# Kernel tuning notes

Hardware: AMD Instinct MI355X
Metric: run time of the kernel (lower is better)

Reference implementation:

```python
import jax, jax.numpy as jnp
import numpy as np

D_MODEL = 256
D_STATE = 64
D_CONV = 4
EXPAND = 2
HEADDIM = 128
CHUNK = 128
D_INNER = EXPAND * D_MODEL            # 512
NHEADS = D_INNER // HEADDIM           # 4
CONV_DIM = D_INNER + 2 * D_STATE      # 640
D_IN_PROJ = 2 * D_INNER + 2 * D_STATE + NHEADS  # 1156
B = 4
H_IMG, W_IMG = 256, 512


def setup_inputs() -> dict:
    key = jax.random.key(0)
    ks = jax.random.split(key, 8)
    rng = np.random.default_rng(0)
    # dt_bias init as in Mamba2: inverse-softplus of dt ~ logU(dt_min, dt_max)
    dt = np.exp(rng.uniform(size=NHEADS) * (np.log(0.1) - np.log(0.001)) + np.log(0.001))
    inv_dt = (dt + np.log(-np.expm1(-dt))).astype(np.float32)
    A_log = np.log(rng.uniform(1.0, 16.0, size=NHEADS)).astype(np.float32)
    return {
        "left_img": jax.random.normal(ks[0], (B, 3, H_IMG, W_IMG), jnp.float32),
        "right_img": jax.random.normal(ks[1], (B, 3, H_IMG, W_IMG), jnp.float32),
        "downsample_w": jax.random.normal(ks[2], (D_MODEL, 3, 4, 4), jnp.float32) * 0.1,
        "downsample_b": jnp.zeros((D_MODEL,), jnp.float32),
        "in_proj_w": jax.random.normal(ks[3], (D_IN_PROJ, D_MODEL), jnp.float32) * (1.0 / np.sqrt(D_MODEL)),
        "conv_w": jax.random.normal(ks[4], (CONV_DIM, 1, D_CONV), jnp.float32) * 0.2,
        "conv_b": jnp.zeros((CONV_DIM,), jnp.float32),
        "dt_bias": jnp.asarray(inv_dt),
        "A_log": jnp.asarray(A_log),
        "D": jnp.ones((NHEADS,), jnp.float32),
        "norm_w": jnp.ones((D_INNER,), jnp.float32),
        "out_proj_w": jax.random.normal(ks[5], (D_MODEL, D_INNER), jnp.float32) * (1.0 / np.sqrt(D_INNER)),
    }


def _ssd_chunk_scan(x, dt, A, Bm, Cm, D):
    """Mamba2 SSD chunked selective scan.
    x: (b,L,H,P), dt: (b,L,H), A: (H,), Bm/Cm: (b,L,N) (ngroups=1), D: (H,).
    Recurrence: h_t = exp(A*dt_t) h_{t-1} + dt_t B_t x_t^T ; y_t = C_t h_t + D x_t.
    """
    b, L, H, P = x.shape
    N = Bm.shape[-1]
    nc = L // CHUNK
    x_ = x.reshape(b, nc, CHUNK, H, P)
    dt_ = dt.reshape(b, nc, CHUNK, H)
    B_ = Bm.reshape(b, nc, CHUNK, N)
    C_ = Cm.reshape(b, nc, CHUNK, N)
    a = dt_ * A                                   # (b,nc,Q,H)
    cum = jnp.cumsum(a, axis=2)                   # (b,nc,Q,H)
    # intra-chunk (causal) contribution
    seg = cum[:, :, :, None, :] - cum[:, :, None, :, :]   # (b,nc,Q,Q,H)
    tril = jnp.tril(jnp.ones((CHUNK, CHUNK), bool))
    Lmat = jnp.where(tril[None, None, :, :, None], jnp.exp(seg), 0.0)
    CB = jnp.einsum('bcin,bcjn->bcij', C_, B_)
    scores = CB[..., None] * Lmat * dt_[:, :, None, :, :]  # (b,nc,Q,Q,H)
    y = jnp.einsum('bcijh,bcjhp->bcihp', scores, x_)
    # per-chunk end states
    decay_to_end = jnp.exp(cum[:, :, -1:, :] - cum)        # (b,nc,Q,H)
    states = jnp.einsum('bcjn,bcjh,bcjhp->bchpn', B_, dt_ * decay_to_end, x_)
    chunk_decay = jnp.exp(cum[:, :, -1, :])                # (b,nc,H)
    def step(hprev, inp):
        dec, st = inp
        hnew = hprev * dec[:, :, None, None] + st
        return hnew, hprev  # emit state BEFORE this chunk
    h0 = jnp.zeros((b, H, P, N), x.dtype)
    _, hprevs = jax.lax.scan(step, h0, (jnp.moveaxis(chunk_decay, 1, 0), jnp.moveaxis(states, 1, 0)))
    hprev = jnp.moveaxis(hprevs, 0, 1)                     # (b,nc,H,P,N)
    y = y + jnp.einsum('bcin,bcih,bchpn->bcihp', C_, jnp.exp(cum), hprev)
    y = y + D[None, None, None, :, None] * x_
    return y.reshape(b, L, H, P)


def reference(left_img, right_img, downsample_w, downsample_b, in_proj_w, conv_w,
              conv_b, dt_bias, A_log, D, norm_w, out_proj_w):
    def downsample(img):
        y = jax.lax.conv_general_dilated(img, downsample_w, (4, 4), 'VALID',
                                         dimension_numbers=('NCHW', 'OIHW', 'NCHW'))
        return y + downsample_b[None, :, None, None]

    ld = downsample(left_img)   # (b, d_model, 64, 128)
    rd = downsample(right_img)
    b, c, h, w = ld.shape
    L = h * w
    lf = ld.transpose(0, 2, 3, 1).reshape(b, L, c)
    rf = rd.transpose(0, 2, 3, 1).reshape(b, L, c)

    zxl = lf @ in_proj_w.T
    zxr = rf @ in_proj_w.T

    def split_proj(zx):
        z = zx[..., :D_INNER]
        xBC = zx[..., D_INNER:D_INNER + CONV_DIM]
        dt = jax.nn.softplus(zx[..., D_INNER + CONV_DIM:] + dt_bias)
        return z, xBC, dt

    zl, xBCl, dtl = split_proj(zxl)
    zr, xBCr, dtr = split_proj(zxr)

    # causal depthwise conv + SiLU applied to LEFT stream only (as in source)
    xt = xBCl.transpose(0, 2, 1)  # (b, conv_dim, L)
    yt = jax.lax.conv_general_dilated(xt, conv_w, (1,), [(D_CONV - 1, 0)],
                                      dimension_numbers=('NCH', 'OIH', 'NCH'),
                                      feature_group_count=CONV_DIM)
    xBCl = jax.nn.silu((yt + conv_b[None, :, None]).transpose(0, 2, 1))

    def split_xbc(xBC):
        return (xBC[..., :D_INNER],
                xBC[..., D_INNER:D_INNER + D_STATE],
                xBC[..., D_INNER + D_STATE:])

    xl, Bl, Cl = split_xbc(xBCl)
    xr, Br, Cr = split_xbc(xBCr)

    A = -jnp.exp(A_log)
    heads = lambda x: x.reshape(b, L, NHEADS, HEADDIM)
    # cross-mixed scans (faithful to source)
    yl = _ssd_chunk_scan(heads(xr), dtl, A, Br, Cl, D).reshape(b, L, D_INNER)
    yr = _ssd_chunk_scan(heads(xl), dtr, A, Bl, Cr, D).reshape(b, L, D_INNER)

    def gated_rmsnorm(y, z):
        y = y * jax.nn.silu(z)
        return y * jax.lax.rsqrt(jnp.mean(y * y, axis=-1, keepdims=True) + 1e-5) * norm_w

    out_l = (gated_rmsnorm(yl, zl) @ out_proj_w.T).reshape(b, h, w, c)
    out_r = (gated_rmsnorm(yr, zr) @ out_proj_w.T).reshape(b, h, w, c)
    return out_l, out_r
```

## Files before the change

### kernel.cpp

```cpp
#include <hip/hip_runtime.h>
#include <hip/hip_fp16.h>
#include <math.h>


typedef _Float16 f16;
typedef __attribute__((ext_vector_type(8))) _Float16 f16x8;
typedef __attribute__((ext_vector_type(4))) _Float16 f16x4;
typedef __attribute__((ext_vector_type(4))) float f32x4;

__device__ __forceinline__ float fexpf(float v) { return __expf(v); }
__device__ __forceinline__ float siluf(float v) { return v / (1.0f + __expf(-v)); }

__device__ __forceinline__ void gload_lds16(const void* g, void* l) {
    __builtin_amdgcn_global_load_lds(
        (const __attribute__((address_space(1))) void*)g,
        (__attribute__((address_space(3))) void*)l, 16, 0, 0);
}

__global__ __launch_bounds__(256) void k_cvt(
    const float* __restrict__ s, f16* __restrict__ d, int n)
{
    int i = blockIdx.x * 256 + threadIdx.x;
    if (i < n) d[i] = (f16)s[i];
}

__global__ __launch_bounds__(256) void k_downsample(
    const float* __restrict__ limg, const float* __restrict__ rimg,
    const float* __restrict__ w, const float* __restrict__ bias,
    f16* __restrict__ F)
{
    __shared__ float wS[12288];
    __shared__ float pS[768];
    int t = threadIdx.x;
    int bid = blockIdx.x;
    int og = bid & 7;
    int oy = (bid >> 3) & 63;
    int b  = (bid >> 9) & 3;
    int side = bid >> 11;
    const float* img = side ? rimg : limg;

    for (int e = t * 4; e < 12288; e += 1024)
        *(float4*)(wS + e) = *(const float4*)(w + e);

    int ox0 = og * 16;
    for (int f = t; f < 768; f += 256) {
        int kx = f & 3, pix = (f >> 2) & 15, ky = (f >> 6) & 3, ci = f >> 8;
        float v = img[((b * 3 + ci) * 256 + oy * 4 + ky) * 512 + ox0 * 4 + pix * 4 + kx];
        pS[pix * 48 + ci * 16 + ky * 4 + kx] = v;
    }
    __syncthreads();

    int c = t;
    float wreg[48];
#pragma unroll
    for (int q = 0; q < 12; q++) {
        float4 v = *(const float4*)(wS + c * 48 + q * 4);
        wreg[q * 4 + 0] = v.x; wreg[q * 4 + 1] = v.y;
        wreg[q * 4 + 2] = v.z; wreg[q * 4 + 3] = v.w;
    }
    float bv = bias[c];
    long base = ((long)(side * 32768 + b * 8192 + oy * 128 + ox0)) * 256 + c;
    for (int pix = 0; pix < 16; pix++) {
        float acc = bv;
#pragma unroll
        for (int q = 0; q < 12; q++) {
            float4 p4 = *(const float4*)(pS + pix * 48 + q * 4);
            acc += wreg[q * 4 + 0] * p4.x + wreg[q * 4 + 1] * p4.y
                 + wreg[q * 4 + 2] * p4.z + wreg[q * 4 + 3] * p4.w;
        }
        F[base + (long)pix * 256] = (f16)acc;
    }
}

template<typename TO>
__global__ __launch_bounds__(256) void k_gemm_mfma(
    const f16* __restrict__ A, const f16* __restrict__ B,
    TO* __restrict__ CL, TO* __restrict__ CR, int K, int ldc, int split)
{
    __shared__ f16 As[128 * 64];
    __shared__ f16 Bs[128 * 64];
    int t = threadIdx.x;
    int w = t >> 6, lane = t & 63;
    int wm = w >> 1, wn = w & 1;

    int gx = gridDim.x, gy = gridDim.y;
    int nwg = gx * gy;
    int orig = blockIdx.y * gx + blockIdx.x;
    int swz = (orig & 7) * (nwg >> 3) + (orig >> 3);
    int mt, nt;
    if (gx <= gy) { mt = swz % gx; nt = swz / gx; }
    else          { nt = swz % gy; mt = swz / gy; }
    long m0 = (long)mt * 128;
    int n0 = nt * 128;

    f32x4 acc[4][4] = {};

    const f16* ga = A + (m0 + w * 8 + (lane >> 3)) * K + (lane & 7) * 8;
    const f16* gb = B + ((long)n0 + w * 8 + (lane >> 3)) * K + (lane & 7) * 8;
    f16* la = As + (w * 8) * 64;
    f16* lb = Bs + (w * 8) * 64;

    for (int kk = 0; kk < K; kk += 64) {
#pragma unroll
        for (int i = 0; i < 4; i++) {
            gload_lds16(ga + (long)i * 32 * K + kk, la + i * 32 * 64);
            gload_lds16(gb + (long)i * 32 * K + kk, lb + i * 32 * 64);
        }
        __syncthreads();

        const f16* pa = As + (wm * 64 + (lane & 15)) * 64 + (lane >> 4) * 8;
        const f16* pb = Bs + (wn * 64 + (lane & 15)) * 64 + (lane >> 4) * 8;
#pragma unroll
        for (int kb = 0; kb < 2; kb++) {
            f16x8 af[4], bf[4];
#pragma unroll
            for (int r = 0; r < 4; r++)
                af[r] = *(const f16x8*)(pa + r * 16 * 64 + kb * 32);
#pragma unroll
            for (int cn = 0; cn < 4; cn++)
                bf[cn] = *(const f16x8*)(pb + cn * 16 * 64 + kb * 32);
#pragma unroll
            for (int r = 0; r < 4; r++)
#pragma unroll
                for (int cn = 0; cn < 4; cn++)
                    acc[r][cn] = __builtin_amdgcn_mfma_f32_16x16x32_f16(
                        af[r], bf[cn], acc[r][cn], 0, 0, 0);
        }
        __syncthreads();
    }

    int rb = (lane >> 4) * 4;
    int cb = lane & 15;
#pragma unroll
    for (int r = 0; r < 4; r++) {
        long mrow = m0 + wm * 64 + r * 16 + rb;
#pragma unroll
        for (int reg = 0; reg < 4; reg++) {
            long row = mrow + reg;
            TO* Cp = (row < split) ? CL + row * ldc : CR + (row - split) * ldc;
#pragma unroll
            for (int cn = 0; cn < 4; cn++)
                Cp[n0 + wn * 64 + cn * 16 + cb] = (TO)acc[r][cn][reg];
        }
    }
}

__global__ __launch_bounds__(256) void k_dt(
    const f16* __restrict__ F, const float* __restrict__ W,
    const float* __restrict__ dt_bias, float* __restrict__ dtbuf)
{
    int t = threadIdx.x;
    int wv = t >> 6, lane = t & 63;
    long m = (long)blockIdx.x * 4 + wv;
    f16x4 fv = *(const f16x4*)(F + m * 256 + lane * 4);
    float dots[4];
#pragma unroll
    for (int h = 0; h < 4; h++) {
        float4 w4 = *(const float4*)(W + (long)(1152 + h) * 256 + lane * 4);
        float d = (float)fv[0] * w4.x + (float)fv[1] * w4.y
                + (float)fv[2] * w4.z + (float)fv[3] * w4.w;
#pragma unroll
        for (int off = 32; off; off >>= 1) d += __shfl_down(d, off, 64);
        dots[h] = d;
    }
    if (lane == 0) {
        long sb = m >> 13;
        long l = m & 8191;
#pragma unroll
        for (int h = 0; h < 4; h++) {
            float v = dots[h] + dt_bias[h];
            float sp = (v > 20.0f) ? v : log1pf(expf(v));
            dtbuf[(sb * 4 + h) * 8192 + l] = sp;
        }
    }
}

__global__ __launch_bounds__(256) void k_cum(
    const float* __restrict__ dtbuf, const float* __restrict__ A_log,
    float* __restrict__ cumbuf, float* __restrict__ wbuf)
{
    int wv = threadIdx.x >> 6, lane = threadIdx.x & 63;
    int g = blockIdx.x * 4 + wv;
    int c = g & 63, h = (g >> 6) & 3, sb = g >> 8;
    float A = -__expf(A_log[h]);
    long base = ((long)sb * 4 + h) * 8192 + c * 128;
    float2 d = *(const float2*)(dtbuf + base + lane * 2);
    float a0 = d.x * A;
    float p = a0 + d.y * A;
    float s = p;
#pragma unroll
    for (int off = 1; off < 64; off <<= 1) {
        float v = __shfl_up(s, off, 64);
        if (lane >= off) s += v;
    }
    float excl = s - p;
    float c0 = excl + a0, c1 = excl + p;
    float cl = __shfl(s, 63, 64);
    *(float2*)(cumbuf + base + lane * 2) = make_float2(c0, c1);
    *(float2*)(wbuf + base + lane * 2) =
        make_float2(d.x * __expf(cl - c0), d.y * __expf(cl - c1));
}

__global__ __launch_bounds__(256) void k_conv_x(
    const f16* __restrict__ xT, const float* __restrict__ cw,
    const float* __restrict__ cb, f16* __restrict__ XCt)
{
    int bid = blockIdx.x;
    int c = bid >> 4;
    int b = (bid >> 2) & 3;
    int tile = bid & 3;
    int l0 = tile * 2048 + threadIdx.x * 8;
    const f16* row = xT + (long)c * 65536 + b * 8192;
    float w0 = cw[c * 4 + 0], w1 = cw[c * 4 + 1],
          w2 = cw[c * 4 + 2], w3 = cw[c * 4 + 3];
    float bv = cb[c];
    float xv[11];
    f16x8 v = *(const f16x8*)(row + l0);
#pragma unroll
    for (int q = 0; q < 8; q++) xv[3 + q] = (float)v[q];
    if (l0 > 0) {
        xv[0] = (float)row[l0 - 3];
        xv[1] = (float)row[l0 - 2];
        xv[2] = (float)row[l0 - 1];
    } else { xv[0] = xv[1] = xv[2] = 0.f; }
    f16x8 o;
#pragma unroll
    for (int q = 0; q < 8; q++) {
        float acc = bv + w0 * xv[q] + w1 * xv[q + 1] + w2 * xv[q + 2] + w3 * xv[q + 3];
        o[q] = (f16)siluf(acc);
    }
    *(f16x8*)(XCt + (long)c * 32768 + b * 8192 + l0) = o;
}

__global__ __launch_bounds__(256) void k_conv_bc(
    const f16* __restrict__ bcLr, const float* __restrict__ cw,
    const float* __restrict__ cb, f16* __restrict__ bcL)
{
    long idx = (long)blockIdx.x * 256 + threadIdx.x;
    int n = (int)(idx & 127);
    long m = idx >> 7;
    int l = (int)(m & 8191);
    float acc = cb[512 + n];
#pragma unroll
    for (int k = 0; k < 4; k++) {
        int j = l - 3 + k;
        if (j >= 0) acc += cw[(512 + n) * 4 + k] * (float)bcLr[(m - 3 + k) * 128 + n];
    }
    bcL[m * 128 + n] = (f16)siluf(acc);
}

__global__ __launch_bounds__(256) void k_ssd_a(
    const f16* __restrict__ xT, const f16* __restrict__ XCt,
    const f16* __restrict__ bcR, const f16* __restrict__ bcL,
    const float* __restrict__ dtbuf, const float* __restrict__ cumbuf,
    const float* __restrict__ wbuf, const float* __restrict__ Dvec,
    f16* __restrict__ ybuf, f16* __restrict__ states)
{
    extern __shared__ f16 sm[];
    f16* Xs = sm;
    f16* Cs = sm + 16384;
    f16* Bs = sm + 24576;
    f16* Ms = sm + 16384;

    int t = threadIdx.x;
    int w = t >> 6, lane = t & 63;
    int quad = lane >> 4, l16 = lane & 15;
    int wm = w >> 1, wn = w & 1;
    int bid = blockIdx.x;
    int side = bid >> 10, rem = bid & 1023;
    int b = rem >> 8, c = (rem >> 2) & 63, h = rem & 3;
    long l0 = (long)b * 8192 + c * 128;
    long dtbase = ((long)(side * 4 + b) * 4 + h) * 8192 + c * 128;

    const f16* Xg; long ldx;
    const f16 *Bg, *Cg;
    if (side == 0) {
        Xg = xT + (long)(h * 128) * 65536 + 32768 + l0; ldx = 65536;
        Bg = bcR + l0 * 128;
        Cg = bcL + l0 * 128 + 64;
    } else {
        Xg = XCt + (long)(h * 128) * 32768 + l0;        ldx = 32768;
        Bg = bcL + l0 * 128;
        Cg = bcR + l0 * 128 + 64;
    }

    int sw8 = l16 & 7;

#pragma unroll
    for (int q = 0; q < 8; q++) {
        int r0 = w * 32 + q * 4;
        int R = r0 + quad;
        gload_lds16(Xg + (long)R * ldx + ((l16 ^ (R & 7)) << 3), Xs + r0 * 128);
    }
#pragma unroll
    for (int q = 0; q < 4; q++) {
        int r0 = w * 32 + q * 8;
        int R = r0 + (lane >> 3);
        int cc = ((lane & 7) ^ (R & 7)) << 3;
        gload_lds16(Cg + (long)R * 128 + cc, Cs + r0 * 64);
        gload_lds16(Bg + (long)R * 128 + cc, Bs + r0 * 64);
    }

    float cum_i[16], cum_j[4], dt_j[4];
#pragma unroll
    for (int r = 0; r < 4; r++)
#pragma unroll
        for (int reg = 0; reg < 4; reg++)
            cum_i[r * 4 + reg] = cumbuf[dtbase + wm * 64 + r * 16 + quad * 4 + reg];
#pragma unroll
    for (int cn = 0; cn < 4; cn++) {
        int j = wn * 64 + cn * 16 + l16;
        cum_j[cn] = cumbuf[dtbase + j];
        dt_j[cn] = dtbuf[dtbase + j];
    }
    float Dh = Dvec[h];
    __syncthreads();

    f32x4 g[4][4] = {};
#pragma unroll
    for (int kb = 0; kb < 2; kb++) {
        f16x8 af[4], bf[4];
#pragma unroll
        for (int r = 0; r < 4; r++)
            af[r] = *(const f16x8*)(Cs + (wm * 64 + r * 16 + l16) * 64
                                       + (((quad + kb * 4) ^ sw8) << 3));
#pragma unroll
        for (int cn = 0; cn < 4; cn++)
            bf[cn] = *(const f16x8*)(Bs + (wn * 64 + cn * 16 + l16) * 64
                                        + (((quad + kb * 4) ^ sw8) << 3));
#pragma unroll
        for (int r = 0; r < 4; r++)
#pragma unroll
            for (int cn = 0; cn < 4; cn++)
                g[r][cn] = __builtin_amdgcn_mfma_f32_16x16x32_f16(
                    af[r], bf[cn], g[r][cn], 0, 0, 0);
    }
    __syncthreads();

#pragma unroll
    for (int r = 0; r < 4; r++)
#pragma unroll
        for (int cn = 0; cn < 4; cn++)
#pragma unroll
            for (int reg = 0; reg < 4; reg++) {
                int i = wm * 64 + r * 16 + quad * 4 + reg;
                int j = wn * 64 + cn * 16 + l16;
                float v = 0.f;
                if (i >= j)
                    v = g[r][cn][reg] * fexpf(cum_i[r * 4 + reg] - cum_j[cn]) * dt_j[cn];
                if (i == j) v += Dh;
                Ms[i * 128 + ((((j >> 3) ^ (i & 7))) << 3) + (j & 7)] = (f16)v;
            }
    __syncthreads();

    f32x4 y[4][4] = {};
#pragma unroll
    for (int kb = 0; kb < 4; kb++) {
        f16x8 af[4], bf[4];
#pragma unroll
        for (int r = 0; r < 4; r++)
            af[r] = *(const f16x8*)(Ms + (wm * 64 + r * 16 + l16) * 128
                                       + (((quad + kb * 4) ^ sw8) << 3));
#pragma unroll
        for (int cn = 0; cn < 4; cn++)
            bf[cn] = *(const f16x8*)(Xs + (wn * 64 + cn * 16 + l16) * 128
                                        + (((quad + kb * 4) ^ sw8) << 3));
#pragma unroll
        for (int r = 0; r < 4; r++)
#pragma unroll
            for (int cn = 0; cn < 4; cn++)
                y[r][cn] = __builtin_amdgcn_mfma_f32_16x16x32_f16(
                    af[r], bf[cn], y[r][cn], 0, 0, 0);
    }
    long ybase = (long)side * 32768 + l0;
#pragma unroll
    for (int r = 0; r < 4; r++)
#pragma unroll
        for (int reg = 0; reg < 4; reg++) {
            int i = wm * 64 + r * 16 + quad * 4 + reg;
#pragma unroll
            for (int cn = 0; cn < 4; cn++) {
                int p = wn * 64 + cn * 16 + l16;
                ybuf[(ybase + i) * 512 + h * 128 + p] = (f16)y[r][cn][reg];
            }
        }

    f32x4 s[4][2] = {};
#pragma unroll
    for (int kb = 0; kb < 4; kb++) {
        float wj[8];
#pragma unroll
        for (int jj = 0; jj < 8; jj++)
            wj[jj] = wbuf[dtbase + kb * 32 + quad * 8 + jj];
        f16x8 af[4], bf[2];
#pragma unroll
        for (int r = 0; r < 4; r++)
            af[r] = *(const f16x8*)(Xs + (wm * 64 + r * 16 + l16) * 128
                                       + (((quad + kb * 4) ^ sw8) << 3));
#pragma unroll
        for (int cn = 0; cn < 2; cn++) {
            int n = wn * 32 + cn * 16 + l16;
#pragma unroll
            for (int jj = 0; jj < 8; jj++) {
                int j = kb * 32 + quad * 8 + jj;
                bf[cn][jj] = (f16)((float)Bg[(long)j * 128 + n] * wj[jj]);
            }
        }
#pragma unroll
        for (int r = 0; r < 4; r++)
#pragma unroll
            for (int cn = 0; cn < 2; cn++)
                s[r][cn] = __builtin_amdgcn_mfma_f32_16x16x32_f16(
                    af[r], bf[cn], s[r][cn], 0, 0, 0);
    }
    long sbase = (((long)(side * 4 + b) * 64 + c) * 4 + h) * 128;
#pragma unroll
    for (int r = 0; r < 4; r++)
#pragma unroll
        for (int reg = 0; reg < 4; reg++) {
            int p = wm * 64 + r * 16 + quad * 4 + reg;
#pragma unroll
            for (int cn = 0; cn < 2; cn++) {
                int n = wn * 32 + cn * 16 + l16;
                states[(sbase + p) * 64 + n] = (f16)s[r][cn][reg];
            }
        }
}

__global__ __launch_bounds__(256) void k_scan(
    f16* __restrict__ states, const float* __restrict__ cumbuf)
{
    long g = (long)blockIdx.x * 256 + threadIdx.x;
    int n = (int)(g & 63);
    int p = (int)((g >> 6) & 127);
    int h = (int)((g >> 13) & 3);
    int sb = (int)(g >> 15);
    long sbase = (((long)sb * 256 + h) * 128 + p) * 64 + n;
    long cbase = ((long)sb * 4 + h) * 8192 + 127;
    float hr = 0.f;
    for (int c = 0; c < 64; c++) {
        long idx = sbase + (long)c * 32768;
        float dec = fexpf(cumbuf[cbase + (long)c * 128]);
        float sv = (float)states[idx];
        states[idx] = (f16)hr;
        hr = hr * dec + sv;
    }
}

__global__ __launch_bounds__(256) void k_ssd_c(
    const f16* __restrict__ bcR, const f16* __restrict__ bcL,
    const f16* __restrict__ states, const float* __restrict__ cumbuf,
    f16* __restrict__ ybuf)
{
    int t = threadIdx.x;
    int w = t >> 6, lane = t & 63;
    int quad = lane >> 4, l16 = lane & 15;
    int wm = w >> 1, wn = w & 1;
    int bid = blockIdx.x;
    int side = bid >> 10, rem = bid & 1023;
    int b = rem >> 8, c = (rem >> 2) & 63, h = rem & 3;
    long l0 = (long)b * 8192 + c * 128;
    long dtbase = ((long)(side * 4 + b) * 4 + h) * 8192 + c * 128;

    const f16* Cg = (side == 0) ? bcL + l0 * 128 + 64 : bcR + l0 * 128 + 64;
    long stile = (((long)(side * 4 + b) * 64 + c) * 4 + h) * 8192;

    f32x4 acc[4][4] = {};
#pragma unroll
    for (int kb = 0; kb < 2; kb++) {
        f16x8 af[4], bf[4];
#pragma unroll
        for (int r = 0; r < 4; r++)
            af[r] = *(const f16x8*)(Cg + (long)(wm * 64 + r * 16 + l16) * 128 + quad * 8 + kb * 32);
#pragma unroll
        for (int cn = 0; cn < 4; cn++)
            bf[cn] = *(const f16x8*)(states + stile + (long)(wn * 64 + cn * 16 + l16) * 64 + quad * 8 + kb * 32);
#pragma unroll
        for (int r = 0; r < 4; r++)
#pragma unroll
            for (int cn = 0; cn < 4; cn++)
                acc[r][cn] = __builtin_amdgcn_mfma_f32_16x16x32_f16(
                    af[r], bf[cn], acc[r][cn], 0, 0, 0);
    }
    long ybase = (long)side * 32768 + l0;
#pragma unroll
    for (int r = 0; r < 4; r++)
#pragma unroll
        for (int reg = 0; reg < 4; reg++) {
            int i = wm * 64 + r * 16 + quad * 4 + reg;
            float ex = fexpf(cumbuf[dtbase + i]);
            f16* yrow = ybuf + (ybase + i) * 512 + h * 128;
#pragma unroll
            for (int cn = 0; cn < 4; cn++) {
                int p = wn * 64 + cn * 16 + l16;
                yrow[p] = (f16)((float)yrow[p] + ex * acc[r][cn][reg]);
            }
        }
}

__global__ __launch_bounds__(256) void k_rmsnorm(
    __half* __restrict__ ybuf, const __half* __restrict__ zbuf,
    const float* __restrict__ nw)
{
    int t = threadIdx.x;
    int wv = t >> 6, lane = t & 63;
    long r = (long)blockIdx.x * 4 + wv;
    __half2* yrow = (__half2*)(ybuf + r * 512 + lane * 8);
    const __half2* zrow = (const __half2*)(zbuf + r * 512 + lane * 8);
    float g[8];
#pragma unroll
    for (int j = 0; j < 4; j++) {
        float2 yv = __half22float2(yrow[j]);
        float2 zv = __half22float2(zrow[j]);
        g[2 * j]     = yv.x * siluf(zv.x);
        g[2 * j + 1] = yv.y * siluf(zv.y);
    }
    float ss = 0.f;
#pragma unroll
    for (int i = 0; i < 8; i++) ss += g[i] * g[i];
#pragma unroll
    for (int off = 32; off; off >>= 1) ss += __shfl_xor(ss, off, 64);
    float sc = rsqrtf(ss * (1.0f / 512.0f) + 1e-5f);
#pragma unroll
    for (int j = 0; j < 4; j++) {
        float w0 = nw[lane * 8 + 2 * j], w1 = nw[lane * 8 + 2 * j + 1];
        yrow[j] = __floats2half2_rn(g[2 * j] * sc * w0, g[2 * j + 1] * sc * w1);
    }
}

extern "C" void kernel_launch(void* const* d_in, const int* in_sizes, int n_in,
                              void* d_out, int out_size, void* d_ws, size_t ws_size,
                              hipStream_t stream)
{
    (void)in_sizes; (void)n_in; (void)out_size; (void)ws_size;
    const float* limg = (const float*)d_in[0];
    const float* rimg = (const float*)d_in[1];
    const float* dsw  = (const float*)d_in[2];
    const float* dsb  = (const float*)d_in[3];
    const float* ipw  = (const float*)d_in[4];
    const float* cw   = (const float*)d_in[5];
    const float* cb   = (const float*)d_in[6];
    const float* dtb  = (const float*)d_in[7];
    const float* alog = (const float*)d_in[8];
    const float* Dv   = (const float*)d_in[9];
    const float* nw   = (const float*)d_in[10];
    const float* opw  = (const float*)d_in[11];
    float* out = (float*)d_out;

    char* ws = (char*)d_ws;
    f16*   F16    = (f16*)  (ws + 0);
    f16*   ipw16  = (f16*)  (ws + 33554432);
    f16*   opw16  = (f16*)  (ws + 34146304);
    float* dtbuf  = (float*)(ws + 34408448);
    float* cumbuf = (float*)(ws + 35457024);
    float* wbuf   = (float*)(ws + 36505600);
    f16*   xT     = (f16*)  (ws + 37554176);
    f16*   XCt    = (f16*)  (ws + 104663040);
    f16*   bcLr   = (f16*)  (ws + 138217472);
    f16*   bcR    = (f16*)  (ws + 146606080);
    f16*   bcL    = (f16*)  (ws + 154994688);
    f16*   ybuf   = (f16*)  (ws + 163383296);
    f16*   states = (f16*)  (ws + 230492160);
    f16*   zbuf   = xT;

    const int BIG = 1 << 30;
    k_downsample<<<4096, 256, 0, stream>>>(limg, rimg, dsw, dsb, F16);
    k_cvt<<<1156, 256, 0, stream>>>(ipw, ipw16, 1156 * 256);
    k_cvt<<<512, 256, 0, stream>>>(opw, opw16, 256 * 512);
    k_gemm_mfma<f16><<<dim3(512, 1), 256, 0, stream>>>(
        F16, ipw16 + 1024 * 256, bcLr, bcR, 256, 128, 32768);
    k_gemm_mfma<f16><<<dim3(4, 512), 256, 0, stream>>>(
        ipw16 + 512 * 256, F16, xT, xT, 256, 65536, BIG);
    k_dt<<<16384, 256, 0, stream>>>(F16, ipw, dtb, dtbuf);
    k_cum<<<512, 256, 0, stream>>>(dtbuf, alog, cumbuf, wbuf);
    k_conv_x<<<8192, 256, 0, stream>>>(xT, cw, cb, XCt);
    k_conv_bc<<<16384, 256, 0, stream>>>(bcLr, cw, cb, bcL);
    k_ssd_a<<<2048, 256, 65536, stream>>>(
        xT, XCt, bcR, bcL, dtbuf, cumbuf, wbuf, Dv, ybuf, states);
    k_scan<<<1024, 256, 0, stream>>>(states, cumbuf);
    k_ssd_c<<<2048, 256, 0, stream>>>(bcR, bcL, states, cumbuf, ybuf);
    k_gemm_mfma<f16><<<dim3(512, 4), 256, 0, stream>>>(
        F16, ipw16, zbuf, zbuf, 256, 512, BIG);
    k_rmsnorm<<<16384, 256, 0, stream>>>((__half*)ybuf, (__half*)zbuf, nw);
    k_gemm_mfma<float><<<dim3(512, 2), 256, 0, stream>>>(
        ybuf, opw16, out, out + (long)32768 * 256, 512, 256, 32768);
}
```

Baseline: 504.8 us.

## Fuse inter-chunk state output with gated RMSNorm via LDS-resident y tile

Merges the inter-chunk output kernel and the gated RMSNorm kernel. Each block now loads a 64-row by 512-column y tile into swizzled LDS, adds the state contribution for all four heads there, then applies SiLU gating and the RMSNorm before writing y back once. This removes the read-modify-write global passes over y that the two separate kernels made. The scan kernel also preloads all 64 chunk states into registers before running the recurrence, which raises register pressure. The fused kernel needs 64KB of LDS per block and gives each block less parallelism across heads.

After: 559.1 us. +10.8%, slower.

```diff
diff --git a/kernel.cpp b/kernel.cpp
--- a/kernel.cpp
+++ b/kernel.cpp
@@ -437,94 +437,132 @@
     int sb = (int)(g >> 15);
     long sbase = (((long)sb * 256 + h) * 128 + p) * 64 + n;
     long cbase = ((long)sb * 4 + h) * 8192 + 127;
+    float sv[64];
+#pragma unroll
+    for (int c = 0; c < 64; c++)
+        sv[c] = (float)states[sbase + (long)c * 32768];
     float hr = 0.f;
+#pragma unroll
     for (int c = 0; c < 64; c++) {
-        long idx = sbase + (long)c * 32768;
-        float dec = fexpf(cumbuf[cbase + (long)c * 128]);
-        float sv = (float)states[idx];
-        states[idx] = (f16)hr;
-        hr = hr * dec + sv;
-    }
-}
-
-__global__ __launch_bounds__(256) void k_ssd_c(
+        states[sbase + (long)c * 32768] = (f16)hr;
+        hr = hr * fexpf(cumbuf[cbase + (long)c * 128]) + sv[c];
+    }
+}
+
+__global__ __launch_bounds__(256) void k_ssd_cn(
     const f16* __restrict__ bcR, const f16* __restrict__ bcL,
     const f16* __restrict__ states, const float* __restrict__ cumbuf,
+    const f16* __restrict__ zbuf, const float* __restrict__ nw,
     f16* __restrict__ ybuf)
 {
+    extern __shared__ f16 gS[];
     int t = threadIdx.x;
     int w = t >> 6, lane = t & 63;
     int quad = lane >> 4, l16 = lane & 15;
     int wm = w >> 1, wn = w & 1;
     int bid = blockIdx.x;
-    int side = bid >> 10, rem = bid & 1023;
-    int b = rem >> 8, c = (rem >> 2) & 63, h = rem & 3;
-    long l0 = (long)b * 8192 + c * 128;
-    long dtbase = ((long)(side * 4 + b) * 4 + h) * 8192 + c * 128;
-
-    const f16* Cg = (side == 0) ? bcL + l0 * 128 + 64 : bcR + l0 * 128 + 64;
-    long stile = (((long)(side * 4 + b) * 64 + c) * 4 + h) * 8192;
-
-    f32x4 acc[4][4] = {};
-#pragma unroll
-    for (int kb = 0; kb < 2; kb++) {
-        f16x8 af[4], bf[4];
-#pragma unroll
-        for (int r = 0; r < 4; r++)
-            af[r] = *(const f16x8*)(Cg + (long)(wm * 64 + r * 16 + l16) * 128 + quad * 8 + kb * 32);
-#pragma unroll
-        for (int cn = 0; cn < 4; cn++)
-            bf[cn] = *(const f16x8*)(states + stile + (long)(wn * 64 + cn * 16 + l16) * 64 + quad * 8 + kb * 32);
-#pragma unroll
-        for (int r = 0; r < 4; r++)
+    int sb = bid >> 7, c = (bid >> 1) & 63, half = bid & 1;
+    int side = sb >> 2, b = sb & 3;
+    long lrow0 = (long)b * 8192 + c * 128 + half * 64;
+    long grow0 = (long)side * 32768 + lrow0;
+
+    {
+        int row = t >> 2, quarter = t & 3;
+        const f16* src = ybuf + (grow0 + row) * 512 + quarter * 128;
+        f16* dst = gS + row * 512;
+        int sw = (row & 7) << 3;
+#pragma unroll
+        for (int k = 0; k < 16; k++) {
+            int lg = quarter * 16 + k;
+            *(f16x8*)(dst + ((lg ^ sw) << 3)) = *(const f16x8*)(src + k * 8);
+        }
+    }
+    __syncthreads();
+
+    const f16* Cg = ((side == 0) ? bcL : bcR) + lrow0 * 128 + 64;
+    f16x8 af[2][2];
+#pragma unroll
+    for (int r = 0; r < 2; r++)
+#pragma unroll
+        for (int kb = 0; kb < 2; kb++)
+            af[r][kb] = *(const f16x8*)(Cg + (long)(wm * 32 + r * 16 + l16) * 128
+                                           + quad * 8 + kb * 32);
+#pragma unroll
+    for (int h = 0; h < 4; h++) {
+        long stile = (((long)sb * 64 + c) * 4 + h) * 8192;
+        f32x4 acc[2][4] = {};
+#pragma unroll
+        for (int kb = 0; kb < 2; kb++) {
+            f16x8 bf[4];
 #pragma unroll
             for (int cn = 0; cn < 4; cn++)
-                acc[r][cn] = __builtin_amdgcn_mfma_f32_16x16x32_f16(
-                    af[r], bf[cn], acc[r][cn], 0, 0, 0);
-    }
-    long ybase = (long)side * 32768 + l0;
-#pragma unroll
-    for (int r = 0; r < 4; r++)
-#pragma unroll
-        for (int reg = 0; reg < 4; reg++) {
-            int i = wm * 64 + r * 16 + quad * 4 + reg;
-            float ex = fexpf(cumbuf[dtbase + i]);
-            f16* yrow = ybuf + (ybase + i) * 512 + h * 128;
-#pragma unroll
-            for (int cn = 0; cn < 4; cn++) {
-                int p = wn * 64 + cn * 16 + l16;
-                yrow[p] = (f16)((float)yrow[p] + ex * acc[r][cn][reg]);
+                bf[cn] = *(const f16x8*)(states + stile
+                            + (long)(wn * 64 + cn * 16 + l16) * 64 + quad * 8 + kb * 32);
+#pragma unroll
+            for (int r = 0; r < 2; r++)
+#pragma unroll
+                for (int cn = 0; cn < 4; cn++)
+                    acc[r][cn] = __builtin_amdgcn_mfma_f32_16x16x32_f16(
+                        af[r][kb], bf[cn], acc[r][cn], 0, 0, 0);
+        }
+        long dtb = ((long)sb * 4 + h) * 8192 + c * 128 + half * 64;
+#pragma unroll
+        for (int r = 0; r < 2; r++)
+#pragma unroll
+            for (int reg = 0; reg < 4; reg++) {
+                int i = wm * 32 + r * 16 + quad * 4 + reg;
+                float ex = fexpf(cumbuf[dtb + i]);
+                int sw = (i & 7) << 3;
+#pragma unroll
+                for (int cn = 0; cn < 4; cn++) {
+                    int col = h * 128 + wn * 64 + cn * 16 + l16;
+                    int addr = i * 512 + ((((col >> 3) ^ sw)) << 3) + (col & 7);
+                    gS[addr] = (f16)((float)gS[addr] + ex * acc[r][cn][reg]);
+                }
             }
-        }
-}
-
-__global__ __launch_bounds__(256) void k_rmsnorm(
-    __half* __restrict__ ybuf, const __half* __restrict__ zbuf,
-    const float* __restrict__ nw)
-{
-    int t = threadIdx.x;
-    int wv = t >> 6, lane = t & 63;
-    long r = (long)blockIdx.x * 4 + wv;
-    __half2* yrow = (__half2*)(ybuf + r * 512 + lane * 8);
-    const __half2* zrow = (const __half2*)(zbuf + r * 512 + lane * 8);
-    float g[8];
-#pragma unroll
-    for (int j = 0; j < 4; j++) {
-        float2 yv = __half22float2(yrow[j]);
-        float2 zv = __half22float2(zrow[j]);
-        g[2 * j]     = yv.x * siluf(zv.x);
-        g[2 * j + 1] = yv.y * siluf(zv.y);
-    }
-    float ss = 0.f;
-#pragma unroll
-    for (int i = 0; i < 8; i++) ss += g[i] * g[i];
-#pragma unroll
-    for (int off = 32; off; off >>= 1) ss += __shfl_xor(ss, off, 64);
-    float sc = rsqrtf(ss * (1.0f / 512.0f) + 1e-5f);
-#pragma unroll
-    for (int j = 0; j < 4; j++) {
-        float w0 = nw[lane * 8 + 2 * j], w1 = nw[lane * 8 + 2 * j + 1];
-        yrow[j] = __floats2half2_rn(g[2 * j] * sc * w0, g[2 * j + 1] * sc * w1);
+    }
+    __syncthreads();
+
+    {
+        int row = t >> 2, quarter = t & 3;
+        int sw = (row & 7) << 3;
+        long grow = grow0 + row;
+        const f16* zrow = zbuf + grow * 512 + quarter * 128;
+        f16x8 gv[16];
+        float ssq = 0.f;
+#pragma unroll
+        for (int k = 0; k < 16; k++) {
+            int lg = quarter * 16 + k;
+            f16x8 yv = *(const f16x8*)(gS + row * 512 + ((lg ^ sw) << 3));
+            f16x8 zv = *(const f16x8*)(zrow + k * 8);
+            f16x8 gg;
+#pragma unroll
+            for (int q = 0; q < 8; q++) {
+                float gf = (float)yv[q] * siluf((float)zv[q]);
+                gg[q] = (f16)gf;
+                ssq += gf * gf;
+            }
+            gv[k] = gg;
+        }
+        ssq += __shfl_xor(ssq, 1, 64);
+        ssq += __shfl_xor(ssq, 2, 64);
+        float sc = rsqrtf(ssq * (1.0f / 512.0f) + 1e-5f);
+        f16* orow = ybuf + grow * 512 + quarter * 128;
+#pragma unroll
+        for (int k = 0; k < 16; k++) {
+            float4 w0 = *(const float4*)(nw + quarter * 128 + k * 8);
+            float4 w1 = *(const float4*)(nw + quarter * 128 + k * 8 + 4);
+            f16x8 o;
+            o[0] = (f16)((float)gv[k][0] * sc * w0.x);
+            o[1] = (f16)((float)gv[k][1] * sc * w0.y);
+            o[2] = (f16)((float)gv[k][2] * sc * w0.z);
+            o[3] = (f16)((float)gv[k][3] * sc * w0.w);
+            o[4] = (f16)((float)gv[k][4] * sc * w1.x);
+            o[5] = (f16)((float)gv[k][5] * sc * w1.y);
+            o[6] = (f16)((float)gv[k][6] * sc * w1.z);
+            o[7] = (f16)((float)gv[k][7] * sc * w1.w);
+            *(f16x8*)(orow + k * 8) = o;
+        }
     }
 }
 
@@ -578,10 +616,10 @@
     k_ssd_a<<<2048, 256, 65536, stream>>>(
         xT, XCt, bcR, bcL, dtbuf, cumbuf, wbuf, Dv, ybuf, states);
     k_scan<<<1024, 256, 0, stream>>>(states, cumbuf);
-    k_ssd_c<<<2048, 256, 0, stream>>>(bcR, bcL, states, cumbuf, ybuf);
     k_gemm_mfma<f16><<<dim3(512, 4), 256, 0, stream>>>(
         F16, ipw16, zbuf, zbuf, 256, 512, BIG);
-    k_rmsnorm<<<16384, 256, 0, stream>>>((__half*)ybuf, (__half*)zbuf, nw);
+    k_ssd_cn<<<1024, 256, 65536, stream>>>(
+        bcR, bcL, states, cumbuf, zbuf, nw, ybuf);
     k_gemm_mfma<float><<<dim3(512, 2), 256, 0, stream>>>(
         ybuf, opw16, out, out + (long)32768 * 256, 512, 256, 32768);
 }
```
